# Optimization experiments

Measured on AMD Instinct MI355X. Metric: run time of the kernel, lower is better.

## Reference

```python
import jax, jax.numpy as jnp
import numpy as np

B, SEQ_LEN, CHANNELS, PRED_LEN = 64, 1024, 512, 720
KERNEL = 25
PAD = (KERNEL - 1) // 2  # 12
IN_LEN = SEQ_LEN // 2    # 512
INV_SQRT2 = 1.0 / np.sqrt(2.0).astype(np.float32)


def dct2_ortho_matrix(N):
    # Orthonormal DCT-II basis: X_k = s_k * sum_n x_n cos(pi*(n+0.5)*k/N)
    n = np.arange(N, dtype=np.float64)
    k = np.arange(N, dtype=np.float64)
    M = np.cos(np.pi * (n[None, :] + 0.5) * k[:, None] / N)
    scale = np.sqrt(2.0 / N) * np.ones(N)
    scale[0] = np.sqrt(1.0 / N)
    return jnp.asarray((scale[:, None] * M).astype(np.float32))  # [k, n]


def setup_inputs() -> dict:
    key = jax.random.key(0)
    k1, k2, k3, k4, k5 = jax.random.split(key, 5)
    bound = 1.0 / np.sqrt(IN_LEN)
    return {
        "x": jax.random.normal(k1, (B, SEQ_LEN, CHANNELS), dtype=jnp.float32),
        "W_seasonal": jax.random.uniform(k2, (PRED_LEN, IN_LEN), jnp.float32, -bound, bound),
        "b_seasonal": jax.random.uniform(k3, (PRED_LEN,), jnp.float32, -bound, bound),
        "W_trend": jax.random.uniform(k4, (PRED_LEN, IN_LEN), jnp.float32, -bound, bound),
        "b_trend": jax.random.uniform(k5, (PRED_LEN,), jnp.float32, -bound, bound),
    }


def reference(x, W_seasonal, b_seasonal, W_trend, b_trend):
    # --- series decomposition: moving average (edge-padded, window 25) ---
    padded = jnp.pad(x, ((0, 0), (PAD, PAD), (0, 0)), mode="edge")  # [B, L+24, C]
    cs = jnp.cumsum(padded, axis=1)
    cs = jnp.pad(cs, ((0, 0), (1, 0), (0, 0)))  # leading zero, [B, L+25, C]
    trend = (cs[:, KERNEL:, :] - cs[:, :-KERNEL, :]) / KERNEL  # [B, L, C]
    seasonal = x - trend

    # [B, C, L]
    s = jnp.transpose(seasonal, (0, 2, 1))
    t = jnp.transpose(trend, (0, 2, 1))

    # --- grouped conv1d with [1,1]/sqrt(2), stride 2 (Haar low-pass downsample) ---
    def down(v):
        return (v[..., 0::2] + v[..., 1::2]) * INV_SQRT2  # [B, C, L/2]

    s = down(s)
    t = down(t)

    # --- orthonormal DCT-II over last axis, then divide by length ---
    Mdct = dct2_ortho_matrix(IN_LEN)  # [k, n]
    s = jnp.einsum("bcn,kn->bck", s, Mdct) / IN_LEN
    t = jnp.einsum("bcn,kn->bck", t, Mdct) / IN_LEN

    # --- shared Linear per branch ---
    s_out = jnp.einsum("bck,pk->bcp", s, W_seasonal) + b_seasonal
    t_out = jnp.einsum("bck,pk->bcp", t, W_trend) + b_trend

    out = s_out + t_out  # [B, C, pred_len]
    return jnp.transpose(out, (0, 2, 1))  # [B, pred_len, C]
```

## Files before the change

kernel.cpp:

```cpp
#include <hip/hip_runtime.h>
#include <hip/hip_bf16.h>
#include <math.h>


#define BATCH 64
#define SEQ 1024
#define CH 512
#define PRED 720
#define INV_SQRT2 0.70710678118654752440f

typedef __attribute__((ext_vector_type(4))) float floatx4;
typedef __attribute__((ext_vector_type(8))) short bf16x8;

#define KBF_OFF   0ull
#define BIAS_OFF  1572864ull
#define WEFFS_OFF 2624512ull
#define WEFFT_OFF 4099072ull
#define XT_OFF    5573632ull
#define WS_NEED   (XT_OFF + 67108864ull)

__device__ __forceinline__ void async_ld16(const void* g, void* l) {
    __builtin_amdgcn_global_load_lds((const __attribute__((address_space(1))) void*)g,
                                     (__attribute__((address_space(3))) void*)l, 16, 0, 0);
}

__device__ __forceinline__ short f2bf(float f) {
    __hip_bfloat16 h = __float2bfloat16(f);
    return *reinterpret_cast<short*>(&h);
}

__global__ void __launch_bounds__(256) xpose(const float* __restrict__ x,
                                             short* __restrict__ xT) {
    __shared__ float lds[64][65];
    int t = threadIdx.x;
    int l0 = blockIdx.x * 64, c0 = blockIdx.y * 64, b = blockIdx.z;
    const float* xb = x + (size_t)b * SEQ * CH;
    int row4 = t >> 4, cq = t & 15;
#pragma unroll
    for (int i = 0; i < 4; i++) {
        int row = row4 + i * 16;
        floatx4 v = *reinterpret_cast<const floatx4*>(
            xb + (size_t)(l0 + row) * CH + c0 + cq * 4);
#pragma unroll
        for (int e = 0; e < 4; e++) lds[row][cq * 4 + e] = v[e];
    }
    __syncthreads();
    size_t outb = (size_t)b * CH * SEQ;
#pragma unroll
    for (int r = 0; r < 2; r++) {
        int u = r * 256 + t;
        int lr = u & 7, c = u >> 3;
        bf16x8 s;
#pragma unroll
        for (int e = 0; e < 8; e++) s[e] = f2bf(lds[lr * 8 + e][c]);
        *reinterpret_cast<bf16x8*>(&xT[outb + (size_t)(c0 + c) * SEQ + l0 + lr * 8]) = s;
    }
}

__global__ void __launch_bounds__(256) build_weff(
    const float* __restrict__ Ws_in, const float* __restrict__ Wt_in,
    float* __restrict__ outS, float* __restrict__ outT) {
    const float* W = blockIdx.z ? Wt_in : Ws_in;
    float* out     = blockIdx.z ? outT  : outS;
    int n0 = blockIdx.x * 64;
    int p0 = blockIdx.y * 64;
    int t  = threadIdx.x;
    int tx = t & 15, ty = t >> 4;
    __shared__ float wlds[32][65];
    __shared__ float mlds[32][64];
    float a[4][4] = {};
    for (int kb = 0; kb < 512; kb += 32) {
        __syncthreads();
        {
            int pp = t >> 2, kk0 = (t & 3) * 8;
            int prow = min(p0 + pp, PRED - 1);
            const float* wsrc = &W[(size_t)prow * 512 + kb + kk0];
#pragma unroll
            for (int e = 0; e < 8; e++) wlds[kk0 + e][pp] = wsrc[e];
        }
        {
            int kk = t >> 3, nn0 = (t & 7) * 8;
            int k = kb + kk;
            float scale = (k == 0) ? 0.04419417382415922f : 0.0625f;
            scale *= (1.0f / 512.0f);
#pragma unroll
            for (int e = 0; e < 8; e++) {
                int n = n0 + nn0 + e;
                int m = ((2 * n + 1) * k) & 2047;
                float ang = (float)m * (float)(M_PI / 1024.0);
                mlds[kk][nn0 + e] = cosf(ang) * scale;
            }
        }
        __syncthreads();
#pragma unroll
        for (int kk = 0; kk < 32; kk++) {
            floatx4 wv = *reinterpret_cast<const floatx4*>(&wlds[kk][ty * 4]);
            floatx4 mv = *reinterpret_cast<const floatx4*>(&mlds[kk][tx * 4]);
#pragma unroll
            for (int i = 0; i < 4; i++)
#pragma unroll
                for (int j = 0; j < 4; j++)
                    a[i][j] += wv[i] * mv[j];
        }
    }
#pragma unroll
    for (int i = 0; i < 4; i++) {
        int p = p0 + ty * 4 + i;
        if (p < PRED) {
            floatx4 v = {a[i][0], a[i][1], a[i][2], a[i][3]};
            *reinterpret_cast<floatx4*>(&out[(size_t)p * 512 + n0 + tx * 4]) = v;
        }
    }
}

__device__ __forceinline__ int tcnt(int j, int l) {
    if (l == 0)    return max(0, 13 - j);
    if (l == 1023) return max(0, j - 1010);
    int d = l - j; if (d < 0) d = -d;
    return (d <= 12) ? 1 : 0;
}

__global__ void build_kmat(const float* __restrict__ Ws, const float* __restrict__ Wt,
                           const float* __restrict__ bs, const float* __restrict__ bt,
                           __hip_bfloat16* __restrict__ Kbf, float* __restrict__ bias) {
    int idx = blockIdx.x * 256 + threadIdx.x;
    int p = idx >> 10, l = idx & 1023;
    if (p >= PRED) { Kbf[idx] = __float2bfloat16(0.0f); return; }
    if (l == 0) bias[p] = bs[p] + bt[p];
    float v = INV_SQRT2 * Ws[(size_t)p * 512 + (l >> 1)];
    int jlo = max(0, l - 12), jhi = min(1023, l + 12);
    float acc = 0.f;
    for (int n = (jlo >> 1); n <= (jhi >> 1); n++) {
        int c = tcnt(2 * n, l) + tcnt(2 * n + 1, l);
        if (c) acc += (Wt[(size_t)p * 512 + n] - Ws[(size_t)p * 512 + n]) * (float)c;
    }
    v += acc * (INV_SQRT2 / 25.0f);
    Kbf[idx] = __float2bfloat16(v);
}

__global__ void __launch_bounds__(512, 2) gemm_main_t(
    const short* __restrict__ Kbf, const short* __restrict__ xT,
    const float* __restrict__ bias, float* __restrict__ out) {
    __shared__ __align__(16) short ldsbuf[2 * 32768];
    int t = threadIdx.x;
    int wave = t >> 6, lane = t & 63;
    int bid = blockIdx.x;
    int work = (bid & 7) * 48 + (bid >> 3);
    int mt = work % 3;
    int nt = work / 3;
    int wm = wave >> 2, wn = wave & 3;
    const short* Ag = Kbf + (size_t)mt * 256 * 1024;
    const short* Bg = xT + (size_t)nt * 256 * 1024;

    size_t so[4];
#pragma unroll
    for (int a = 0; a < 4; a++) {
        int s = a * 512 + t;
        so[a] = (size_t)(((s >> 7) << 4) + (s & 15)) * 1024
              + ((s >> 6) & 1) * 32 + ((s >> 4) & 3) * 8;
    }

    floatx4 acc[8][4];
#pragma unroll
    for (int i = 0; i < 8; i++)
#pragma unroll
        for (int j = 0; j < 4; j++)
            acc[i][j] = (floatx4){0.f, 0.f, 0.f, 0.f};

#define STAGE(bufidx, k0v)                                                     \
    {                                                                          \
        char* base_ = (char*)ldsbuf + (bufidx) * 65536;                        \
        _Pragma("unroll")                                                      \
        for (int a = 0; a < 4; a++)                                            \
            async_ld16(Ag + so[a] + (k0v), base_ + a * 8192 + wave * 1024);    \
        _Pragma("unroll")                                                      \
        for (int a = 0; a < 4; a++)                                            \
            async_ld16(Bg + so[a] + (k0v),                                     \
                       base_ + 32768 + a * 8192 + wave * 1024);                \
    }

#define COMPUTE(cbp)                                                           \
    {                                                                          \
        _Pragma("unroll")                                                      \
        for (int ks = 0; ks < 2; ks++) {                                       \
            bf16x8 af[8], bf[4];                                               \
            _Pragma("unroll")                                                  \
            for (int i = 0; i < 8; i++)                                        \
                af[i] = *reinterpret_cast<const bf16x8*>(                      \
                    (cbp) + ((wm * 8 + i) << 11) + (ks << 10) + (lane << 4));  \
            _Pragma("unroll")                                                  \
            for (int j = 0; j < 4; j++)                                        \
                bf[j] = *reinterpret_cast<const bf16x8*>(                      \
                    (cbp) + 32768 + ((wn * 4 + j) << 11) + (ks << 10) +        \
                    (lane << 4));                                              \
            __builtin_amdgcn_s_setprio(1);                                     \
            _Pragma("unroll")                                                  \
            for (int i = 0; i < 8; i++)                                        \
                _Pragma("unroll")                                              \
                for (int j = 0; j < 4; j++)                                    \
                    acc[i][j] = __builtin_amdgcn_mfma_f32_16x16x32_bf16(       \
                        af[i], bf[j], acc[i][j], 0, 0, 0);                     \
            __builtin_amdgcn_s_setprio(0);                                     \
        }                                                                      \
    }

    STAGE(0, 0);
    STAGE(1, 64);

    for (int it = 0; it < 15; ++it) {
        asm volatile("s_waitcnt vmcnt(8)" ::: "memory");
        __builtin_amdgcn_s_barrier();
        __builtin_amdgcn_sched_barrier(0);
        const char* cbp = (const char*)ldsbuf + (it & 1) * 65536;
        COMPUTE(cbp);
        __builtin_amdgcn_sched_barrier(0);
        __builtin_amdgcn_s_barrier();
        __builtin_amdgcn_sched_barrier(0);
        if (it < 14) STAGE(it & 1, (it + 2) * 64);
    }
    asm volatile("s_waitcnt vmcnt(0)" ::: "memory");
    __builtin_amdgcn_s_barrier();
    __builtin_amdgcn_sched_barrier(0);
    {
        const char* cbp = (const char*)ldsbuf + 65536;
        COMPUTE(cbp);
    }
#undef STAGE
#undef COMPUTE

    int lm = lane & 15, kq = lane >> 4;
    int p0r = mt * 256 + wm * 128;
    int b   = nt >> 1;
    int cb2 = (nt & 1) * 256 + wn * 64 + lm;
    size_t outb = (size_t)b * PRED * CH;
#pragma unroll
    for (int i = 0; i < 8; i++) {
#pragma unroll
        for (int r = 0; r < 4; r++) {
            int p = p0r + i * 16 + kq * 4 + r;
            if (p < PRED) {
                float bv = bias[p];
#pragma unroll
                for (int j = 0; j < 4; j++)
                    __builtin_nontemporal_store(acc[i][j][r] + bv,
                                                &out[outb + (size_t)p * CH + cb2 + j * 16]);
            }
        }
    }
}

__global__ void __launch_bounds__(256) gemm_main(
    const short* __restrict__ Kbf, const float* __restrict__ x,
    const float* __restrict__ bias, float* __restrict__ out) {
    __shared__ __align__(16) short ldsA[128 * 32];
    int t = threadIdx.x;
    int wave = t >> 6, lane = t & 63;
    int mt = blockIdx.x % 6, nt = blockIdx.x / 6;
    int b  = blockIdx.y;
    int wm = wave >> 1, wn = wave & 1;
    const short* Ag = Kbf + (size_t)mt * 128 * 1024;
    const float* xb = x + (size_t)b * SEQ * CH;
    int lm = lane & 15, kq = lane >> 4;
    int cj[4];
    for (int j = 0; j < 4; j++) cj[j] = nt * 128 + wn * 64 + j * 16 + lm;

    floatx4 acc[4][4];
    for (int i = 0; i < 4; i++)
        for (int j = 0; j < 4; j++)
            acc[i][j] = (floatx4){0.f, 0.f, 0.f, 0.f};

    for (int k0 = 0; k0 < 1024; k0 += 32) {
        for (int rdi = 0; rdi < 2; rdi++) {
            int q = rdi * 256 + t;
            int row = q >> 2, ko = (q & 3) * 8;
            async_ld16(Ag + (size_t)row * 1024 + k0 + ko,
                       (char*)ldsA + rdi * 4096 + wave * 1024);
        }
        bf16x8 bfrag[4];
        int krow = k0 + kq * 8;
#pragma unroll
        for (int j = 0; j < 4; j++) {
            const float* xc = xb + (size_t)krow * CH + cj[j];
            bf16x8 bv;
#pragma unroll
            for (int i = 0; i < 8; i++) bv[i] = f2bf(xc[(size_t)i * CH]);
            bfrag[j] = bv;
        }
        __syncthreads();
        bf16x8 af[4];
        for (int i = 0; i < 4; i++)
            af[i] = *(const bf16x8*)&ldsA[(wm * 64 + i * 16 + lm) * 32 + kq * 8];
        for (int i = 0; i < 4; i++)
            for (int j = 0; j < 4; j++)
                acc[i][j] = __builtin_amdgcn_mfma_f32_16x16x32_bf16(af[i], bfrag[j], acc[i][j], 0, 0, 0);
        __syncthreads();
    }

    int p0 = mt * 128 + wm * 64;
    size_t outb = (size_t)b * PRED * CH;
    for (int i = 0; i < 4; i++) {
        for (int r = 0; r < 4; r++) {
            int p = p0 + i * 16 + kq * 4 + r;
            if (p < PRED) {
                float bv = bias[p];
                for (int j = 0; j < 4; j++) {
                    out[outb + (size_t)p * CH + cj[j]] = acc[i][j][r] + bv;
                }
            }
        }
    }
}

extern "C" void kernel_launch(void* const* d_in, const int* in_sizes, int n_in,
                              void* d_out, int out_size, void* d_ws, size_t ws_size,
                              hipStream_t stream) {
    const float* xp = nullptr; const float* wp[2] = {nullptr, nullptr};
    const float* bp[2] = {nullptr, nullptr};
    int wn = 0, bn = 0;
    for (int i = 0; i < n_in; i++) {
        if (in_sizes[i] == 33554432) xp = (const float*)d_in[i];
        else if (in_sizes[i] == 368640 && wn < 2) wp[wn++] = (const float*)d_in[i];
        else if (in_sizes[i] == 720 && bn < 2) bp[bn++] = (const float*)d_in[i];
    }
    if (!xp || wn != 2 || bn != 2) {
        xp = (const float*)d_in[0]; wp[0] = (const float*)d_in[1];
        bp[0] = (const float*)d_in[2]; wp[1] = (const float*)d_in[3];
        bp[1] = (const float*)d_in[4];
    }
    float* out = (float*)d_out;

    char* ws = (char*)d_ws;
    __hip_bfloat16* Kbf = (__hip_bfloat16*)(ws + KBF_OFF);
    float* bias  = (float*)(ws + BIAS_OFF);
    float* WeffS = (float*)(ws + WEFFS_OFF);
    float* WeffT = (float*)(ws + WEFFT_OFF);
    short* xT    = (short*)(ws + XT_OFF);

    bool big = (ws_size >= (size_t)WS_NEED);

    if (big) xpose<<<dim3(16, 8, 64), 256, 0, stream>>>(xp, xT);
    build_weff<<<dim3(8, 12, 2), 256, 0, stream>>>(wp[0], wp[1], WeffS, WeffT);
    build_kmat<<<3072, 256, 0, stream>>>(WeffS, WeffT, bp[0], bp[1], Kbf, bias);
    if (big)
        gemm_main_t<<<384, 512, 0, stream>>>((const short*)Kbf, (const short*)xT, bias, out);
    else
        gemm_main<<<dim3(24, 64), 256, 0, stream>>>((const short*)Kbf, xp, bias, out);
}
```

Baseline: 362.4 us.

## Split GEMM k-step into four phases interleaving LDS reads, async loads, and MFMA

Restructures the main bf16 GEMM loop so each 64-wide k-step is broken into four quadrant phases. Each phase reads a slice of A/B fragments from LDS, issues a portion of the next step's global-to-LDS async loads, then runs a 4x2 block of MFMAs between barriers. This spreads memory traffic across the compute rather than bunching all staging at the end of each iteration, and reduces live fragment registers. The cost is more barriers per step and more intricate buffer-reuse timing, where a mistake could cause a race.

```diff
diff --git a/kernel.cpp b/kernel.cpp
--- a/kernel.cpp
+++ b/kernel.cpp
@@ -167,66 +167,136 @@
         for (int j = 0; j < 4; j++)
             acc[i][j] = (floatx4){0.f, 0.f, 0.f, 0.f};
 
-#define STAGE(bufidx, k0v)                                                     \
+    bf16x8 af[4][2], bf[4][2];
+
+#define MFMA16(I0, J0)                                                         \
+    __builtin_amdgcn_s_setprio(1);                                             \
+    _Pragma("unroll")                                                          \
+    for (int i = 0; i < 4; i++)                                                \
+        _Pragma("unroll")                                                      \
+        for (int j = 0; j < 2; j++)                                            \
+            _Pragma("unroll")                                                  \
+            for (int ks = 0; ks < 2; ks++)                                     \
+                acc[(I0) + i][(J0) + j] =                                      \
+                    __builtin_amdgcn_mfma_f32_16x16x32_bf16(                   \
+                        af[i][ks], bf[(J0) + j][ks],                           \
+                        acc[(I0) + i][(J0) + j], 0, 0, 0);                     \
+    __builtin_amdgcn_s_setprio(0);
+
+#define PH_BAR()                                                               \
+    __builtin_amdgcn_s_barrier();                                              \
+    asm volatile("s_waitcnt lgkmcnt(0)" ::: "memory");                         \
+    __builtin_amdgcn_sched_barrier(0);
+
+#define PH_END()                                                               \
+    __builtin_amdgcn_s_barrier();                                              \
+    __builtin_amdgcn_sched_barrier(0);
+
+#define GROUP(G, S123, S4, TAILMODE)                                           \
     {                                                                          \
-        char* base_ = (char*)ldsbuf + (bufidx) * 65536;                        \
+        const char* cb = (const char*)ldsbuf + ((G) & 1) * 65536;              \
+        char* nb = (char*)ldsbuf + (((G) + 1) & 1) * 65536;                    \
+        char* s2 = (char*)ldsbuf + ((G) & 1) * 65536;                          \
+                                    \
         _Pragma("unroll")                                                      \
-        for (int a = 0; a < 4; a++)                                            \
-            async_ld16(Ag + so[a] + (k0v), base_ + a * 8192 + wave * 1024);    \
+        for (int i = 0; i < 4; i++)                                            \
+            _Pragma("unroll")                                                  \
+            for (int ks = 0; ks < 2; ks++)                                     \
+                af[i][ks] = *reinterpret_cast<const bf16x8*>(                  \
+                    cb + ((wm * 8 + i) << 11) + (ks << 10) + (lane << 4));     \
         _Pragma("unroll")                                                      \
-        for (int a = 0; a < 4; a++)                                            \
-            async_ld16(Bg + so[a] + (k0v),                                     \
-                       base_ + 32768 + a * 8192 + wave * 1024);                \
-    }
-
-#define COMPUTE(cbp)                                                           \
-    {                                                                          \
+        for (int j = 0; j < 2; j++)                                            \
+            _Pragma("unroll")                                                  \
+            for (int ks = 0; ks < 2; ks++)                                     \
+                bf[j][ks] = *reinterpret_cast<const bf16x8*>(                  \
+                    cb + 32768 + ((wn * 4 + j) << 11) + (ks << 10) +           \
+                    (lane << 4));                                              \
+        if (S123) {                                                            \
+            async_ld16(Ag + so[2] + ((G) + 1) * 64,                            \
+                       nb + 2 * 8192 + wave * 1024);                           \
+            async_ld16(Ag + so[3] + ((G) + 1) * 64,                            \
+                       nb + 3 * 8192 + wave * 1024);                           \
+        }                                                                      \
+        PH_BAR()                                                               \
+        MFMA16(0, 0)                                                           \
+        PH_END()                                                               \
+                                              \
         _Pragma("unroll")                                                      \
-        for (int ks = 0; ks < 2; ks++) {                                       \
-            bf16x8 af[8], bf[4];                                               \
+        for (int j = 2; j < 4; j++)                                            \
             _Pragma("unroll")                                                  \
-            for (int i = 0; i < 8; i++)                                        \
-                af[i] = *reinterpret_cast<const bf16x8*>(                      \
-                    (cbp) + ((wm * 8 + i) << 11) + (ks << 10) + (lane << 4));  \
+            for (int ks = 0; ks < 2; ks++)                                     \
+                bf[j][ks] = *reinterpret_cast<const bf16x8*>(                  \
+                    cb + 32768 + ((wn * 4 + j) << 11) + (ks << 10) +           \
+                    (lane << 4));                                              \
+        if (S123) {                                                            \
+            async_ld16(Bg + so[0] + ((G) + 1) * 64,                            \
+                       nb + 32768 + 0 * 8192 + wave * 1024);                   \
+            async_ld16(Bg + so[1] + ((G) + 1) * 64,                            \
+                       nb + 32768 + 1 * 8192 + wave * 1024);                   \
+        }                                                                      \
+        PH_BAR()                                                               \
+        MFMA16(0, 2)                                                           \
+        PH_END()                                                               \
+                                 \
+        _Pragma("unroll")                                                      \
+        for (int i = 0; i < 4; i++)                                            \
             _Pragma("unroll")                                                  \
-            for (int j = 0; j < 4; j++)                                        \
-                bf[j] = *reinterpret_cast<const bf16x8*>(                      \
-                    (cbp) + 32768 + ((wn * 4 + j) << 11) + (ks << 10) +        \
-                    (lane << 4));                                              \
-            __builtin_amdgcn_s_setprio(1);                                     \
-            _Pragma("unroll")                                                  \
-            for (int i = 0; i < 8; i++)                                        \
-                _Pragma("unroll")                                              \
-                for (int j = 0; j < 4; j++)                                    \
-                    acc[i][j] = __builtin_amdgcn_mfma_f32_16x16x32_bf16(       \
-                        af[i], bf[j], acc[i][j], 0, 0, 0);                     \
-            __builtin_amdgcn_s_setprio(0);                                     \
+            for (int ks = 0; ks < 2; ks++)                                     \
+                af[i][ks] = *reinterpret_cast<const bf16x8*>(                  \
+                    cb + ((wm * 8 + 4 + i) << 11) + (ks << 10) + (lane << 4)); \
+        if (S123) {                                                            \
+            async_ld16(Bg + so[2] + ((G) + 1) * 64,                            \
+                       nb + 32768 + 2 * 8192 + wave * 1024);                   \
+            async_ld16(Bg + so[3] + ((G) + 1) * 64,                            \
+                       nb + 32768 + 3 * 8192 + wave * 1024);                   \
         }                                                                      \
-    }
-
-    STAGE(0, 0);
-    STAGE(1, 64);
-
-    for (int it = 0; it < 15; ++it) {
-        asm volatile("s_waitcnt vmcnt(8)" ::: "memory");
+        PH_BAR()                                                               \
+        MFMA16(4, 2)                                                           \
+        PH_END()                                                               \
+           \
+            \
+        if (S4) {                                                              \
+            async_ld16(Ag + so[0] + ((G) + 2) * 64,                            \
+                       s2 + 0 * 8192 + wave * 1024);                           \
+            async_ld16(Ag + so[1] + ((G) + 2) * 64,                            \
+                       s2 + 1 * 8192 + wave * 1024);                           \
+        }                                                                      \
+        MFMA16(4, 0)                                                           \
+        if ((TAILMODE) == 2) {                                                 \
+            asm volatile("s_waitcnt vmcnt(2)" ::: "memory");                   \
+            __builtin_amdgcn_s_barrier();                                      \
+            __builtin_amdgcn_sched_barrier(0);                                 \
+        } else if ((TAILMODE) == 0) {                                          \
+            asm volatile("s_waitcnt vmcnt(0)" ::: "memory");                   \
+            __builtin_amdgcn_s_barrier();                                      \
+            __builtin_amdgcn_sched_barrier(0);                                 \
+        }                                                                      \
+    }
+
+    {
+        char* b0 = (char*)ldsbuf;
+        char* b1 = (char*)ldsbuf + 65536;
+#pragma unroll
+        for (int a = 0; a < 4; a++)
+            async_ld16(Ag + so[a], b0 + a * 8192 + wave * 1024);
+#pragma unroll
+        for (int a = 0; a < 4; a++)
+            async_ld16(Bg + so[a], b0 + 32768 + a * 8192 + wave * 1024);
+        async_ld16(Ag + so[0] + 64, b1 + 0 * 8192 + wave * 1024);
+        async_ld16(Ag + so[1] + 64, b1 + 1 * 8192 + wave * 1024);
+        asm volatile("s_waitcnt vmcnt(2)" ::: "memory");
         __builtin_amdgcn_s_barrier();
         __builtin_amdgcn_sched_barrier(0);
-        const char* cbp = (const char*)ldsbuf + (it & 1) * 65536;
-        COMPUTE(cbp);
-        __builtin_amdgcn_sched_barrier(0);
-        __builtin_amdgcn_s_barrier();
-        __builtin_amdgcn_sched_barrier(0);
-        if (it < 14) STAGE(it & 1, (it + 2) * 64);
-    }
-    asm volatile("s_waitcnt vmcnt(0)" ::: "memory");
-    __builtin_amdgcn_s_barrier();
-    __builtin_amdgcn_sched_barrier(0);
-    {
-        const char* cbp = (const char*)ldsbuf + 65536;
-        COMPUTE(cbp);
-    }
-#undef STAGE
-#undef COMPUTE
+    }
+
+    for (int g = 0; g < 14; ++g) GROUP(g, 1, 1, 2);
+    GROUP(14, 1, 0, 0)
+    GROUP(15, 0, 0, -1)
+
+#undef GROUP
+#undef PH_BAR
+#undef PH_END
+#undef MFMA16
 
     int lm = lane & 15, kq = lane >> 4;
     int p0r = mt * 256 + wm * 128;
```

Result: no change. 356.1 us (-1.7%).
